# Kernel tuning notes

Hardware: AMD Instinct MI355X
Metric: run time of the kernel (lower is better)

Reference implementation:

```python
import jax, jax.numpy as jnp
import numpy as np

N = 100000        # nodes
E = 3200000       # edges (avg degree 32)
IN, HID, OUT = 512, 256, 64
K = 10
ALPHA = 0.1


def setup_inputs() -> dict:
    key = jax.random.key(0)
    k1, k2, k3, k4 = jax.random.split(key, 4)
    x = jax.random.normal(k1, (N, IN), dtype=jnp.float32)
    edge_index = jax.random.randint(k2, (2, E), 0, N, dtype=jnp.int64)
    W1 = jax.random.normal(k3, (IN, HID), dtype=jnp.float32) * (1.0 / np.sqrt(IN))
    b1 = jnp.zeros((HID,), dtype=jnp.float32)
    W2 = jax.random.normal(k4, (HID, OUT), dtype=jnp.float32) * (1.0 / np.sqrt(HID))
    b2 = jnp.zeros((OUT,), dtype=jnp.float32)
    return {"x": x, "edge_index": edge_index, "W1": W1, "b1": b1, "W2": W2, "b2": b2}


def reference(x, edge_index, W1, b1, W2, b2):
    # MLP head: Linear -> ReLU -> Linear
    h = jax.nn.relu(x @ W1 + b1)
    h = h @ W2 + b2                                   # [N, OUT]

    # gcn_norm with self-loops: D^-1/2 (A + I) D^-1/2
    src = jnp.concatenate([edge_index[0], jnp.arange(N, dtype=edge_index.dtype)])
    dst = jnp.concatenate([edge_index[1], jnp.arange(N, dtype=edge_index.dtype)])
    deg = jax.ops.segment_sum(jnp.ones_like(src, dtype=h.dtype), dst, num_segments=N)
    dinv = jnp.where(deg > 0, jax.lax.rsqrt(deg), 0.0)
    norm = dinv[src] * dinv[dst]                      # [E+N]

    h0 = h

    def step(h, _):
        msg = h[src] * norm[:, None]                  # gather + edge scale
        agg = jax.ops.segment_sum(msg, dst, num_segments=N)  # scatter-add
        h = (1.0 - ALPHA) * agg + ALPHA * h0          # teleport
        return h, None

    h, _ = jax.lax.scan(step, h, None, length=K)
    return h
```

## Files before the change

### kernel.cpp

```cpp
#include <hip/hip_runtime.h>
#include <hip/hip_bf16.h>
#include <hip/hip_fp16.h>


typedef __bf16 bf16x8 __attribute__((ext_vector_type(8)));
typedef float f32x4 __attribute__((ext_vector_type(4)));

static constexpr int IN = 512, HID = 256, OUT = 64;
static constexpr int LDT = 40;

static __device__ __forceinline__ ushort f2bf(float f) {
  __hip_bfloat16 b = __float2bfloat16(f);
  return *reinterpret_cast<ushort*>(&b);
}
static __device__ __forceinline__ float bf2f(ushort u) {
  unsigned int x = ((unsigned int)u) << 16;
  return __uint_as_float(x);
}
static __device__ __forceinline__ float h15f(unsigned int u) {
  ushort hb = (ushort)(u & 0x7FFFu);
  __half h = *reinterpret_cast<__half*>(&hb);
  return __half2float(h);
}

static __device__ __forceinline__ void gload16(const void* g, void* l) {
  __builtin_amdgcn_global_load_lds(
      (const __attribute__((address_space(1))) void*)g,
      (__attribute__((address_space(3))) void*)l, 16, 0, 0);
}

__global__ void transpose_f32_bf16(const float* __restrict__ in, ushort* __restrict__ out,
                                   int K, int C) {
  int idx = blockIdx.x * 256 + threadIdx.x;
  if (idx < K * C) {
    int n = idx / K, k = idx % K;
    out[idx] = f2bf(in[k * C + n]);
  }
}

__global__ __launch_bounds__(256) void gemm1(const float* __restrict__ X,
                                             const ushort* __restrict__ W1T,
                                             const float* __restrict__ b1,
                                             ushort* __restrict__ h1, int M) {
  __shared__ __align__(16) float As[2][128 * 32];
  __shared__ __align__(16) ushort Bs[2][128 * 32];
  const int tid = threadIdx.x;
  const int m0 = blockIdx.y * 128;
  const int n0 = blockIdx.x * 128;
  const int lane = tid & 63, w = tid >> 6;
  const int wr = w >> 1, wc = w & 1;
  const int lm = lane & 15, lq = lane >> 4;
  const int wbase = w * 64;

  auto STAGE = [&](int k0, int buf) {
#pragma unroll
    for (int i = 0; i < 4; ++i) {
      int idx = i * 256 + tid;
      int row = idx >> 3, ch = idx & 7;
      int gm = m0 + row; gm = gm < M ? gm : M - 1;
      int sch = ch ^ (row & 7);
      gload16(&X[(size_t)gm * IN + k0 + sch * 4], &As[buf][(i * 256 + wbase) * 4]);
    }
#pragma unroll
    for (int i = 0; i < 2; ++i) {
      int idx = i * 256 + tid;
      int row = idx >> 2, ch = idx & 3;
      int sch = ch ^ ((row ^ (row >> 2)) & 3);
      gload16(&W1T[(size_t)(n0 + row) * IN + k0 + sch * 8], &Bs[buf][(i * 256 + wbase) * 8]);
    }
  };

  f32x4 acc[4][4] = {};

  STAGE(0, 0);
  __syncthreads();

  int cur = 0;
  for (int k0 = 0; k0 < IN; k0 += 32) {
    if (k0 + 32 < IN) STAGE(k0 + 32, cur ^ 1);

    bf16x8 af[4], bq[4];
#pragma unroll
    for (int mi = 0; mi < 4; ++mi) {
      int r = wr * 64 + mi * 16 + lm;
      int k7 = r & 7;
      float4 x0 = *reinterpret_cast<const float4*>(&As[cur][r * 32 + ((2 * lq) ^ k7) * 4]);
      float4 x1 = *reinterpret_cast<const float4*>(&As[cur][r * 32 + ((2 * lq + 1) ^ k7) * 4]);
      union { ushort u[8]; bf16x8 v; } cv;
      cv.u[0] = f2bf(x0.x); cv.u[1] = f2bf(x0.y); cv.u[2] = f2bf(x0.z); cv.u[3] = f2bf(x0.w);
      cv.u[4] = f2bf(x1.x); cv.u[5] = f2bf(x1.y); cv.u[6] = f2bf(x1.z); cv.u[7] = f2bf(x1.w);
      af[mi] = cv.v;
    }
#pragma unroll
    for (int ni = 0; ni < 4; ++ni) {
      int r = wc * 64 + ni * 16 + lm;
      int key = (r ^ (r >> 2)) & 3;
      bq[ni] = *reinterpret_cast<const bf16x8*>(&Bs[cur][r * 32 + (lq ^ key) * 8]);
    }
#pragma unroll
    for (int mi = 0; mi < 4; ++mi)
#pragma unroll
      for (int ni = 0; ni < 4; ++ni)
        acc[mi][ni] = __builtin_amdgcn_mfma_f32_16x16x32_bf16(af[mi], bq[ni], acc[mi][ni], 0, 0, 0);

    __syncthreads();
    cur ^= 1;
  }

#pragma unroll
  for (int ni = 0; ni < 4; ++ni) {
    int col = n0 + wc * 64 + ni * 16 + lm;
    float bias = b1[col];
#pragma unroll
    for (int mi = 0; mi < 4; ++mi) {
#pragma unroll
      for (int rg = 0; rg < 4; ++rg) {
        int row = m0 + wr * 64 + mi * 16 + lq * 4 + rg;
        if (row < M) {
          float v = acc[mi][ni][rg] + bias;
          v = v > 0.f ? v : 0.f;
          h1[(size_t)row * HID + col] = f2bf(v);
        }
      }
    }
  }
}

__global__ __launch_bounds__(256) void gemm2(const ushort* __restrict__ h1,
                                             const ushort* __restrict__ W2T,
                                             const float* __restrict__ b2,
                                             float* __restrict__ H0f,
                                             ushort* __restrict__ H0b, int M) {
  __shared__ __align__(16) ushort As[128 * LDT];
  __shared__ __align__(16) ushort Bs[64 * LDT];
  const int tid = threadIdx.x;
  const int m0 = blockIdx.x * 128;
  const int lane = tid & 63, w = tid >> 6;
  const int lm = lane & 15, lq = lane >> 4;
  const int c = tid & 3, r = tid >> 2;

  f32x4 acc[2][4] = {};

  for (int k0 = 0; k0 < HID; k0 += 32) {
#pragma unroll
    for (int rr = 0; rr < 2; ++rr) {
      int m = r + rr * 64;
      int gm = m0 + m; gm = gm < M ? gm : M - 1;
      *reinterpret_cast<int4*>(&As[m * LDT + c * 8]) =
          *reinterpret_cast<const int4*>(&h1[(size_t)gm * HID + k0 + c * 8]);
    }
    *reinterpret_cast<int4*>(&Bs[r * LDT + c * 8]) =
        *reinterpret_cast<const int4*>(&W2T[(size_t)r * HID + k0 + c * 8]);
    __syncthreads();
    bf16x8 af[2], bq[4];
#pragma unroll
    for (int mi = 0; mi < 2; ++mi)
      af[mi] = *reinterpret_cast<const bf16x8*>(&As[(w * 32 + mi * 16 + lm) * LDT + lq * 8]);
#pragma unroll
    for (int ni = 0; ni < 4; ++ni)
      bq[ni] = *reinterpret_cast<const bf16x8*>(&Bs[(ni * 16 + lm) * LDT + lq * 8]);
#pragma unroll
    for (int mi = 0; mi < 2; ++mi)
#pragma unroll
      for (int ni = 0; ni < 4; ++ni)
        acc[mi][ni] = __builtin_amdgcn_mfma_f32_16x16x32_bf16(af[mi], bq[ni], acc[mi][ni], 0, 0, 0);
    __syncthreads();
  }

#pragma unroll
  for (int ni = 0; ni < 4; ++ni) {
    int col = ni * 16 + lm;
    float bias = b2[col];
#pragma unroll
    for (int mi = 0; mi < 2; ++mi) {
#pragma unroll
      for (int rg = 0; rg < 4; ++rg) {
        int row = m0 + w * 32 + mi * 16 + lq * 4 + rg;
        if (row < M) {
          float v = acc[mi][ni][rg] + bias;
          H0f[(size_t)row * OUT + col] = v;
          H0b[(size_t)row * OUT + col] = f2bf(v);
        }
      }
    }
  }
}

__global__ void count_deg(const int* __restrict__ ei, int* __restrict__ cnt, int E) {
  int e = blockIdx.x * 256 + threadIdx.x;
  if (e < E) atomicAdd(&cnt[ei[E + e]], 1);
}

__global__ void calc_dinv(const int* __restrict__ cnt, float* __restrict__ dinv, int n) {
  int v = blockIdx.x * 256 + threadIdx.x;
  if (v < n) dinv[v] = rsqrtf((float)cnt[v] + 1.0f);
}

__global__ __launch_bounds__(1024) void scan_kernel(const int* __restrict__ cnt,
                                                    int* __restrict__ offs,
                                                    int* __restrict__ cursor, int n) {
  __shared__ int wsum[16];
  __shared__ int woff[16];
  __shared__ int carry_s;
  const int tid = threadIdx.x;
  const int lane = tid & 63, wid = tid >> 6;
  if (tid == 0) carry_s = 0;
  __syncthreads();
  for (int base = 0; base < n; base += 4096) {
    int i0 = base + tid * 4;
    int x[4];
#pragma unroll
    for (int j = 0; j < 4; ++j) x[j] = (i0 + j < n) ? cnt[i0 + j] : 0;
    int tsum = x[0] + x[1] + x[2] + x[3];
    int val = tsum;
#pragma unroll
    for (int d = 1; d < 64; d <<= 1) {
      int t = __shfl_up(val, d, 64);
      if (lane >= d) val += t;
    }
    if (lane == 63) wsum[wid] = val;
    __syncthreads();
    if (wid == 0) {
      int s = (lane < 16) ? wsum[lane] : 0;
      int sv = s;
#pragma unroll
      for (int d = 1; d < 16; d <<= 1) {
        int t = __shfl_up(sv, d, 64);
        if (lane >= d) sv += t;
      }
      if (lane < 16) woff[lane] = sv - s;
    }
    __syncthreads();
    int excl = carry_s + woff[wid] + (val - tsum);
#pragma unroll
    for (int j = 0; j < 4; ++j) {
      if (i0 + j < n) { offs[i0 + j] = excl; cursor[i0 + j] = excl; }
      excl += x[j];
    }
    __syncthreads();
    if (tid == 1023) carry_s = excl;
    __syncthreads();
  }
  if (tid == 0) offs[n] = carry_s;
}

__global__ void fill_csr(const int* __restrict__ ei, int* __restrict__ cursor,
                         const float* __restrict__ dinv, unsigned int* __restrict__ csr,
                         int E) {
  int e = blockIdx.x * 256 + threadIdx.x;
  if (e < E) {
    int s = ei[e], d = ei[E + e];
    int p = atomicAdd(&cursor[d], 1);
    float w = dinv[s] * dinv[d];
    __half hw = __float2half(w);
    unsigned int hb = *reinterpret_cast<ushort*>(&hw);
    csr[p] = (((unsigned int)s) << 15) | hb;
  }
}

template <bool WRITE_BF>
__global__ __launch_bounds__(256) void prop_step(const float* __restrict__ hinf,
                                                 const ushort* __restrict__ hinb,
                                                 float* __restrict__ houtf,
                                                 ushort* __restrict__ houtb,
                                                 const float* __restrict__ h0,
                                                 const int* __restrict__ offs,
                                                 const unsigned int* __restrict__ csr,
                                                 const float* __restrict__ dinv, int n) {
  int gw = (blockIdx.x * 256 + threadIdx.x) >> 6;
  int lane = threadIdx.x & 63;
  if (gw >= n) return;
  const unsigned int* hin32 = (const unsigned int*)hinb;
  const int c = lane & 31;
  const int half = lane >> 5;
  float alo[8], ahi[8];
#pragma unroll
  for (int k = 0; k < 8; ++k) { alo[k] = 0.f; ahi[k] = 0.f; }
  int e0 = offs[gw], e1 = offs[gw + 1];
  for (int base = e0; base < e1; base += 64) {
    int rem = e1 - base;
    unsigned int my = (lane < rem) ? csr[base + lane] : 0u;
    int cnt = rem < 64 ? rem : 64;
    int cnt32 = (cnt + 31) & ~31;
    for (int j = 0; j < cnt32; j += 32) {
      unsigned int u[16];
#pragma unroll
      for (int k = 0; k < 16; ++k)
        u[k] = (unsigned int)__shfl((int)my, j + 2 * k + half);
      unsigned int v[16];
#pragma unroll
      for (int k = 0; k < 16; ++k)
        v[k] = hin32[(size_t)(u[k] >> 15) * 32 + c];
#pragma unroll
      for (int k = 0; k < 16; ++k) {
        float w = h15f(u[k]);
        float f0 = __uint_as_float(v[k] << 16);
        float f1 = __uint_as_float(v[k] & 0xFFFF0000u);
        alo[k & 7] = fmaf(w, f0, alo[k & 7]);
        ahi[k & 7] = fmaf(w, f1, ahi[k & 7]);
      }
    }
  }
  float a0 = ((alo[0] + alo[1]) + (alo[2] + alo[3])) + ((alo[4] + alo[5]) + (alo[6] + alo[7]));
  float a1 = ((ahi[0] + ahi[1]) + (ahi[2] + ahi[3])) + ((ahi[4] + ahi[5]) + (ahi[6] + ahi[7]));
  a0 += __shfl_xor(a0, 32, 64);
  a1 += __shfl_xor(a1, 32, 64);
  float dv = dinv[gw];
  float2 hf = ((const float2*)hinf)[(size_t)gw * 32 + c];
  float2 h0f = ((const float2*)h0)[(size_t)gw * 32 + c];
  float o0 = 0.9f * (a0 + dv * dv * hf.x) + 0.1f * h0f.x;
  float o1 = 0.9f * (a1 + dv * dv * hf.y) + 0.1f * h0f.y;
  if (half == 0) {
    float2 ov; ov.x = o0; ov.y = o1;
    ((float2*)houtf)[(size_t)gw * 32 + c] = ov;
  } else if (WRITE_BF) {
    unsigned int pk = (unsigned int)f2bf(o0) | ((unsigned int)f2bf(o1) << 16);
    ((unsigned int*)houtb)[(size_t)gw * 32 + c] = pk;
  }
}

extern "C" void kernel_launch(void* const* d_in, const int* in_sizes, int n_in,
                              void* d_out, int out_size, void* d_ws, size_t ws_size,
                              hipStream_t stream) {
  const float* X  = (const float*)d_in[0];
  const int*   EI = (const int*)d_in[1];
  const float* W1 = (const float*)d_in[2];
  const float* b1 = (const float*)d_in[3];
  const float* W2 = (const float*)d_in[4];
  const float* b2 = (const float*)d_in[5];
  float* out = (float*)d_out;

  const int N = in_sizes[0] / IN;
  const int E = in_sizes[1] / 2;

  char* ws = (char*)d_ws;
  size_t o = 0;
  auto alloc = [&](size_t b) {
    char* p = ws + o;
    o = (o + b + 255) & ~(size_t)255;
    return p;
  };
  float*  H0f  = (float*)alloc((size_t)N * OUT * 4);
  ushort* H0b  = (ushort*)alloc((size_t)N * OUT * 2);
  float*  hAf  = (float*)alloc((size_t)N * OUT * 4);
  ushort* hAb  = (ushort*)alloc((size_t)N * OUT * 2);
  float*  hBf  = (float*)alloc((size_t)N * OUT * 4);
  ushort* hBb  = (ushort*)alloc((size_t)N * OUT * 2);
  ushort* h1   = (ushort*)alloc((size_t)N * HID * 2);
  ushort* W1T  = (ushort*)alloc((size_t)IN * HID * 2);
  ushort* W2T  = (ushort*)alloc((size_t)HID * OUT * 2);
  int*    cnt  = (int*)alloc((size_t)N * 4);
  int*    offs = (int*)alloc((size_t)(N + 1) * 4);
  int*    curs = (int*)alloc((size_t)N * 4);
  float*  dinv = (float*)alloc((size_t)N * 4);
  unsigned int* csr = (unsigned int*)alloc((size_t)E * 4);
  (void)ws_size; (void)n_in; (void)out_size;

  transpose_f32_bf16<<<(IN * HID + 255) / 256, 256, 0, stream>>>(W1, W1T, IN, HID);
  transpose_f32_bf16<<<(HID * OUT + 255) / 256, 256, 0, stream>>>(W2, W2T, HID, OUT);

  gemm1<<<dim3(HID / 128, (N + 127) / 128), 256, 0, stream>>>(X, W1T, b1, h1, N);
  gemm2<<<(N + 127) / 128, 256, 0, stream>>>(h1, W2T, b2, H0f, H0b, N);

  hipMemsetAsync(cnt, 0, (size_t)N * 4, stream);
  count_deg<<<(E + 255) / 256, 256, 0, stream>>>(EI, cnt, E);
  calc_dinv<<<(N + 255) / 256, 256, 0, stream>>>(cnt, dinv, N);
  scan_kernel<<<1, 1024, 0, stream>>>(cnt, offs, curs, N);
  fill_csr<<<(E + 255) / 256, 256, 0, stream>>>(EI, curs, dinv, csr, E);

  const int pgrid = (N * OUT + 255) / 256;
  prop_step<true><<<pgrid, 256, 0, stream>>>(H0f, H0b, hAf, hAb, H0f, offs, csr, dinv, N);
  for (int i = 0; i < 4; ++i) {
    prop_step<true><<<pgrid, 256, 0, stream>>>(hAf, hAb, hBf, hBb, H0f, offs, csr, dinv, N);
    prop_step<true><<<pgrid, 256, 0, stream>>>(hBf, hBb, hAf, hAb, H0f, offs, csr, dinv, N);
  }
  prop_step<false><<<pgrid, 256, 0, stream>>>(hAf, hAb, out, nullptr, H0f, offs, csr, dinv, N);
}
```

Before: 1.349 ms.

## Partition CSR by source-index range and process source partitions in lockstep across nodes

Builds the CSR with 8 sub-buckets per destination, keyed by source index range (s>>14), and scans over N*8 counts. Each propagation wave now handles 17 nodes in a persistent grid of 1536 blocks. It walks the source partitions in order so that all waves gather from the same slice of h at roughly the same time, which should improve L2 hit rate. The cost is more register pressure from 34 accumulators, a scan eight times larger, more per-partition loop overhead, and a narrower inner unroll of 4 gathers.

Result: slower. 4.247 ms (+214.8%).

```diff
diff --git a/kernel.cpp b/kernel.cpp
--- a/kernel.cpp
+++ b/kernel.cpp
@@ -8,6 +8,8 @@
 
 static constexpr int IN = 512, HID = 256, OUT = 64;
 static constexpr int LDT = 40;
+static constexpr int NPW = 17;
+static constexpr int PGRID = 1536;
 
 static __device__ __forceinline__ ushort f2bf(float f) {
   __hip_bfloat16 b = __float2bfloat16(f);
@@ -186,14 +188,18 @@
   }
 }
 
-__global__ void count_deg(const int* __restrict__ ei, int* __restrict__ cnt, int E) {
+__global__ void count_deg8(const int* __restrict__ ei, int* __restrict__ cnt8, int E) {
   int e = blockIdx.x * 256 + threadIdx.x;
-  if (e < E) atomicAdd(&cnt[ei[E + e]], 1);
-}
-
-__global__ void calc_dinv(const int* __restrict__ cnt, float* __restrict__ dinv, int n) {
+  if (e < E) {
+    int s = ei[e], d = ei[E + e];
+    atomicAdd(&cnt8[(size_t)d * 8 + (s >> 14)], 1);
+  }
+}
+
+__global__ void calc_dinv(const int* __restrict__ offs8, float* __restrict__ dinv, int n) {
   int v = blockIdx.x * 256 + threadIdx.x;
-  if (v < n) dinv[v] = rsqrtf((float)cnt[v] + 1.0f);
+  if (v < n)
+    dinv[v] = rsqrtf((float)(offs8[(size_t)(v + 1) * 8] - offs8[(size_t)v * 8]) + 1.0f);
 }
 
 __global__ __launch_bounds__(1024) void scan_kernel(const int* __restrict__ cnt,
@@ -206,12 +212,12 @@
   const int lane = tid & 63, wid = tid >> 6;
   if (tid == 0) carry_s = 0;
   __syncthreads();
-  for (int base = 0; base < n; base += 4096) {
-    int i0 = base + tid * 4;
-    int x[4];
-#pragma unroll
-    for (int j = 0; j < 4; ++j) x[j] = (i0 + j < n) ? cnt[i0 + j] : 0;
-    int tsum = x[0] + x[1] + x[2] + x[3];
+  for (int base = 0; base < n; base += 8192) {
+    int i0 = base + tid * 8;
+    int x[8];
+#pragma unroll
+    for (int j = 0; j < 8; ++j) x[j] = (i0 + j < n) ? cnt[i0 + j] : 0;
+    int tsum = ((x[0] + x[1]) + (x[2] + x[3])) + ((x[4] + x[5]) + (x[6] + x[7]));
     int val = tsum;
 #pragma unroll
     for (int d = 1; d < 64; d <<= 1) {
@@ -233,7 +239,7 @@
     __syncthreads();
     int excl = carry_s + woff[wid] + (val - tsum);
 #pragma unroll
-    for (int j = 0; j < 4; ++j) {
+    for (int j = 0; j < 8; ++j) {
       if (i0 + j < n) { offs[i0 + j] = excl; cursor[i0 + j] = excl; }
       excl += x[j];
     }
@@ -244,13 +250,13 @@
   if (tid == 0) offs[n] = carry_s;
 }
 
-__global__ void fill_csr(const int* __restrict__ ei, int* __restrict__ cursor,
+__global__ void fill_csr(const int* __restrict__ ei, int* __restrict__ cursor8,
                          const float* __restrict__ dinv, unsigned int* __restrict__ csr,
                          int E) {
   int e = blockIdx.x * 256 + threadIdx.x;
   if (e < E) {
     int s = ei[e], d = ei[E + e];
-    int p = atomicAdd(&cursor[d], 1);
+    int p = atomicAdd(&cursor8[(size_t)d * 8 + (s >> 14)], 1);
     float w = dinv[s] * dinv[d];
     __half hw = __float2half(w);
     unsigned int hb = *reinterpret_cast<ushort*>(&hw);
@@ -264,58 +270,73 @@
                                                  float* __restrict__ houtf,
                                                  ushort* __restrict__ houtb,
                                                  const float* __restrict__ h0,
-                                                 const int* __restrict__ offs,
+                                                 const int* __restrict__ offs8,
                                                  const unsigned int* __restrict__ csr,
-                                                 const float* __restrict__ dinv, int n) {
-  int gw = (blockIdx.x * 256 + threadIdx.x) >> 6;
-  int lane = threadIdx.x & 63;
-  if (gw >= n) return;
+                                                 const float* __restrict__ dinv,
+                                                 int n, int nw) {
+  const int wv = (blockIdx.x * 256 + threadIdx.x) >> 6;
+  const int lane = threadIdx.x & 63;
   const unsigned int* hin32 = (const unsigned int*)hinb;
   const int c = lane & 31;
   const int half = lane >> 5;
-  float alo[8], ahi[8];
-#pragma unroll
-  for (int k = 0; k < 8; ++k) { alo[k] = 0.f; ahi[k] = 0.f; }
-  int e0 = offs[gw], e1 = offs[gw + 1];
-  for (int base = e0; base < e1; base += 64) {
-    int rem = e1 - base;
-    unsigned int my = (lane < rem) ? csr[base + lane] : 0u;
-    int cnt = rem < 64 ? rem : 64;
-    int cnt32 = (cnt + 31) & ~31;
-    for (int j = 0; j < cnt32; j += 32) {
-      unsigned int u[16];
-#pragma unroll
-      for (int k = 0; k < 16; ++k)
-        u[k] = (unsigned int)__shfl((int)my, j + 2 * k + half);
-      unsigned int v[16];
-#pragma unroll
-      for (int k = 0; k < 16; ++k)
-        v[k] = hin32[(size_t)(u[k] >> 15) * 32 + c];
-#pragma unroll
-      for (int k = 0; k < 16; ++k) {
-        float w = h15f(u[k]);
-        float f0 = __uint_as_float(v[k] << 16);
-        float f1 = __uint_as_float(v[k] & 0xFFFF0000u);
-        alo[k & 7] = fmaf(w, f0, alo[k & 7]);
-        ahi[k & 7] = fmaf(w, f1, ahi[k & 7]);
-      }
-    }
-  }
-  float a0 = ((alo[0] + alo[1]) + (alo[2] + alo[3])) + ((alo[4] + alo[5]) + (alo[6] + alo[7]));
-  float a1 = ((ahi[0] + ahi[1]) + (ahi[2] + ahi[3])) + ((ahi[4] + ahi[5]) + (ahi[6] + ahi[7]));
-  a0 += __shfl_xor(a0, 32, 64);
-  a1 += __shfl_xor(a1, 32, 64);
-  float dv = dinv[gw];
-  float2 hf = ((const float2*)hinf)[(size_t)gw * 32 + c];
-  float2 h0f = ((const float2*)h0)[(size_t)gw * 32 + c];
-  float o0 = 0.9f * (a0 + dv * dv * hf.x) + 0.1f * h0f.x;
-  float o1 = 0.9f * (a1 + dv * dv * hf.y) + 0.1f * h0f.y;
-  if (half == 0) {
-    float2 ov; ov.x = o0; ov.y = o1;
-    ((float2*)houtf)[(size_t)gw * 32 + c] = ov;
-  } else if (WRITE_BF) {
-    unsigned int pk = (unsigned int)f2bf(o0) | ((unsigned int)f2bf(o1) << 16);
-    ((unsigned int*)houtb)[(size_t)gw * 32 + c] = pk;
+  float a0[NPW], a1[NPW];
+#pragma unroll
+  for (int i = 0; i < NPW; ++i) { a0[i] = 0.f; a1[i] = 0.f; }
+
+  for (int p = 0; p < 8; ++p) {
+#pragma unroll
+    for (int i = 0; i < NPW; ++i) {
+      int node = wv + i * nw;
+      if (node < n) {
+        int e0 = offs8[(size_t)node * 8 + p];
+        int e1 = offs8[(size_t)node * 8 + p + 1];
+        for (int base = e0; base < e1; base += 64) {
+          int rem = e1 - base;
+          unsigned int my = (lane < rem) ? csr[base + lane] : 0u;
+          int cnt = rem < 64 ? rem : 64;
+          for (int j = 0; j < cnt; j += 8) {
+            unsigned int u0 = (unsigned int)__shfl((int)my, j + half, 64);
+            unsigned int u1 = (unsigned int)__shfl((int)my, j + 2 + half, 64);
+            unsigned int u2 = (unsigned int)__shfl((int)my, j + 4 + half, 64);
+            unsigned int u3 = (unsigned int)__shfl((int)my, j + 6 + half, 64);
+            unsigned int w0 = hin32[(size_t)(u0 >> 15) * 32 + c];
+            unsigned int w1 = hin32[(size_t)(u1 >> 15) * 32 + c];
+            unsigned int w2 = hin32[(size_t)(u2 >> 15) * 32 + c];
+            unsigned int w3 = hin32[(size_t)(u3 >> 15) * 32 + c];
+            float p0 = h15f(u0), p1 = h15f(u1), p2 = h15f(u2), p3 = h15f(u3);
+            a0[i] = fmaf(p0, __uint_as_float(w0 << 16), a0[i]);
+            a1[i] = fmaf(p0, __uint_as_float(w0 & 0xFFFF0000u), a1[i]);
+            a0[i] = fmaf(p1, __uint_as_float(w1 << 16), a0[i]);
+            a1[i] = fmaf(p1, __uint_as_float(w1 & 0xFFFF0000u), a1[i]);
+            a0[i] = fmaf(p2, __uint_as_float(w2 << 16), a0[i]);
+            a1[i] = fmaf(p2, __uint_as_float(w2 & 0xFFFF0000u), a1[i]);
+            a0[i] = fmaf(p3, __uint_as_float(w3 << 16), a0[i]);
+            a1[i] = fmaf(p3, __uint_as_float(w3 & 0xFFFF0000u), a1[i]);
+          }
+        }
+      }
+    }
+  }
+
+#pragma unroll
+  for (int i = 0; i < NPW; ++i) {
+    int node = wv + i * nw;
+    if (node < n) {
+      float s0 = a0[i] + __shfl_xor(a0[i], 32, 64);
+      float s1 = a1[i] + __shfl_xor(a1[i], 32, 64);
+      float dv = dinv[node];
+      float2 hf = ((const float2*)hinf)[(size_t)node * 32 + c];
+      float2 hh = ((const float2*)h0)[(size_t)node * 32 + c];
+      float o0 = 0.9f * (s0 + dv * dv * hf.x) + 0.1f * hh.x;
+      float o1 = 0.9f * (s1 + dv * dv * hf.y) + 0.1f * hh.y;
+      if (half == 0) {
+        float2 ov; ov.x = o0; ov.y = o1;
+        ((float2*)houtf)[(size_t)node * 32 + c] = ov;
+      } else if (WRITE_BF) {
+        unsigned int pk = (unsigned int)f2bf(o0) | ((unsigned int)f2bf(o1) << 16);
+        ((unsigned int*)houtb)[(size_t)node * 32 + c] = pk;
+      }
+    }
   }
 }
 
@@ -349,9 +370,9 @@
   ushort* h1   = (ushort*)alloc((size_t)N * HID * 2);
   ushort* W1T  = (ushort*)alloc((size_t)IN * HID * 2);
   ushort* W2T  = (ushort*)alloc((size_t)HID * OUT * 2);
-  int*    cnt  = (int*)alloc((size_t)N * 4);
-  int*    offs = (int*)alloc((size_t)(N + 1) * 4);
-  int*    curs = (int*)alloc((size_t)N * 4);
+  int*    cnt8 = (int*)alloc((size_t)N * 8 * 4);
+  int*    offs8 = (int*)alloc((size_t)(N * 8 + 1) * 4);
+  int*    curs8 = (int*)alloc((size_t)N * 8 * 4);
   float*  dinv = (float*)alloc((size_t)N * 4);
   unsigned int* csr = (unsigned int*)alloc((size_t)E * 4);
   (void)ws_size; (void)n_in; (void)out_size;
@@ -362,17 +383,17 @@
   gemm1<<<dim3(HID / 128, (N + 127) / 128), 256, 0, stream>>>(X, W1T, b1, h1, N);
   gemm2<<<(N + 127) / 128, 256, 0, stream>>>(h1, W2T, b2, H0f, H0b, N);
 
-  hipMemsetAsync(cnt, 0, (size_t)N * 4, stream);
-  count_deg<<<(E + 255) / 256, 256, 0, stream>>>(EI, cnt, E);
-  calc_dinv<<<(N + 255) / 256, 256, 0, stream>>>(cnt, dinv, N);
-  scan_kernel<<<1, 1024, 0, stream>>>(cnt, offs, curs, N);
-  fill_csr<<<(E + 255) / 256, 256, 0, stream>>>(EI, curs, dinv, csr, E);
-
-  const int pgrid = (N * OUT + 255) / 256;
-  prop_step<true><<<pgrid, 256, 0, stream>>>(H0f, H0b, hAf, hAb, H0f, offs, csr, dinv, N);
+  hipMemsetAsync(cnt8, 0, (size_t)N * 8 * 4, stream);
+  count_deg8<<<(E + 255) / 256, 256, 0, stream>>>(EI, cnt8, E);
+  scan_kernel<<<1, 1024, 0, stream>>>(cnt8, offs8, curs8, N * 8);
+  calc_dinv<<<(N + 255) / 256, 256, 0, stream>>>(offs8, dinv, N);
+  fill_csr<<<(E + 255) / 256, 256, 0, stream>>>(EI, curs8, dinv, csr, E);
+
+  const int nwv = PGRID * 4;
+  prop_step<true><<<PGRID, 256, 0, stream>>>(H0f, H0b, hAf, hAb, H0f, offs8, csr, dinv, N, nwv);
   for (int i = 0; i < 4; ++i) {
-    prop_step<true><<<pgrid, 256, 0, stream>>>(hAf, hAb, hBf, hBb, H0f, offs, csr, dinv, N);
-    prop_step<true><<<pgrid, 256, 0, stream>>>(hBf, hBb, hAf, hAb, H0f, offs, csr, dinv, N);
-  }
-  prop_step<false><<<pgrid, 256, 0, stream>>>(hAf, hAb, out, nullptr, H0f, offs, csr, dinv, N);
-}
+    prop_step<true><<<PGRID, 256, 0, stream>>>(hAf, hAb, hBf, hBb, H0f, offs8, csr, dinv, N, nwv);
+    prop_step<true><<<PGRID, 256, 0, stream>>>(hBf, hBb, hAf, hAb, H0f, offs8, csr, dinv, N, nwv);
+  }
+  prop_step<false><<<PGRID, 256, 0, stream>>>(hAf, hAb, out, nullptr, H0f, offs8, csr, dinv, N, nwv);
+}
```
